# Kernel optimization log

Hardware: AMD Instinct MI355X
Metric: run time of the kernel (lower is better)

## Reference

```python
import jax, jax.numpy as jnp
import numpy as np

B, IN, H = 4096, 1024, 1024


def setup_inputs() -> dict:
    key = jax.random.key(0)
    ks = jax.random.split(key, 20)
    s_in = 1.0 / np.sqrt(IN)
    s_h = 1.0 / np.sqrt(H)
    def lin(kw, kb, fan_in, scale):
        W = jax.random.uniform(kw, (H, fan_in), jnp.float32, -scale, scale)
        b = jax.random.uniform(kb, (H,), jnp.float32, -scale, scale)
        return W, b
    Wxf, bxf = lin(ks[0], ks[1], IN, s_in)
    Whf, bhf = lin(ks[2], ks[3], H, s_h)
    Wxi, bxi = lin(ks[4], ks[5], IN, s_in)
    Whi, bhi = lin(ks[6], ks[7], H, s_h)
    Wxo, bxo = lin(ks[8], ks[9], IN, s_in)
    Who, bho = lin(ks[10], ks[11], H, s_h)
    Wxc, bxc = lin(ks[12], ks[13], IN, s_in)
    Whc, bhc = lin(ks[14], ks[15], H, s_h)
    x = jax.random.normal(ks[16], (B, IN), jnp.float32)
    c = jax.random.normal(ks[17], (B, H), jnp.float32)
    h = jax.random.normal(ks[18], (B, H), jnp.float32)
    return dict(x=x, c=c, h=h,
                Wxf=Wxf, bxf=bxf, Whf=Whf, bhf=bhf,
                Wxi=Wxi, bxi=bxi, Whi=Whi, bhi=bhi,
                Wxo=Wxo, bxo=bxo, Who=Who, bho=bho,
                Wxc=Wxc, bxc=bxc, Whc=Whc, bhc=bhc)


def reference(x, c, h,
              Wxf, bxf, Whf, bhf,
              Wxi, bxi, Whi, bhi,
              Wxo, bxo, Who, bho,
              Wxc, bxc, Whc, bhc):
    # Fuse the 8 small GEMMs into two batched GEMMs: x @ Wx^T and h @ Wh^T
    # with gate outputs concatenated along the hidden dim [f, i, o, c~].
    Wx = jnp.concatenate([Wxf, Wxi, Wxo, Wxc], axis=0)   # [4H, IN]
    Wh = jnp.concatenate([Whf, Whi, Who, Whc], axis=0)   # [4H, H]
    bx = jnp.concatenate([bxf, bxi, bxo, bxc], axis=0)   # [4H]
    bh = jnp.concatenate([bhf, bhi, bho, bhc], axis=0)   # [4H]
    gates = x @ Wx.T + h @ Wh.T + (bx + bh)              # [B, 4H]
    hs = Wxf.shape[0]
    f = jax.nn.sigmoid(gates[:, 0 * hs:1 * hs])
    i = jax.nn.sigmoid(gates[:, 1 * hs:2 * hs])
    o = jax.nn.sigmoid(gates[:, 2 * hs:3 * hs])
    ctil = jnp.tanh(gates[:, 3 * hs:4 * hs])
    ct = f * c + ctil * i
    ht = jnp.tanh(ct) * o
    return (ct, ht)
```

## Files before the change

kernel.cpp:

```cpp
#include <hip/hip_runtime.h>
#include <hip/hip_bf16.h>
#include <stdint.h>

typedef __hip_bfloat16 bf16;
typedef __attribute__((ext_vector_type(8))) short short8;
typedef __attribute__((ext_vector_type(4))) float floatx4;

#define AS1(p) ((const __attribute__((address_space(1))) void*)(p))
#define AS3(p) ((__attribute__((address_space(3))) void*)(p))

#define M_DIM 4096
#define H_DIM 1024
#define MEG   (1u << 20)
#define LDS_BUF 24576

__device__ __forceinline__ unsigned short f2bf(float f) {
    uint32_t u = __float_as_uint(f);
    uint32_t r = (u + 0x7FFFu + ((u >> 16) & 1u)) >> 16;
    return (unsigned short)r;
}

__device__ __forceinline__ float fast_sigmoid(float v) {
    return 1.0f / (1.0f + __expf(-v));
}
__device__ __forceinline__ float fast_tanh(float v) {
    return 2.0f / (1.0f + __expf(-2.0f * v)) - 1.0f;
}

__global__ __launch_bounds__(256)
void convert_to_bf16(const float* __restrict__ x, const float* __restrict__ h,
                     const float* Wxf, const float* Wxi, const float* Wxo, const float* Wxc,
                     const float* Whf, const float* Whi, const float* Who, const float* Whc,
                     unsigned short* __restrict__ ws)
{
    const uint32_t idx0 = blockIdx.x * 2048u + threadIdx.x * 8u;
    const uint32_t t = blockIdx.x >> 9;
    const float* src;
    uint32_t off;
    if (t < 4u)      { src = x; off = idx0; }
    else if (t < 8u) { src = h; off = idx0 - (4u << 20); }
    else {
        const uint32_t g = t - 8u;
        src = (g == 0) ? Wxf : (g == 1) ? Wxi : (g == 2) ? Wxo : (g == 3) ? Wxc
            : (g == 4) ? Whf : (g == 5) ? Whi : (g == 6) ? Who : Whc;
        off = idx0 & (MEG - 1u);
    }
    const float4 v0 = *(const float4*)(src + off);
    const float4 v1 = *(const float4*)(src + off + 4);
    short8 pk;
    pk[0] = (short)f2bf(v0.x); pk[1] = (short)f2bf(v0.y);
    pk[2] = (short)f2bf(v0.z); pk[3] = (short)f2bf(v0.w);
    pk[4] = (short)f2bf(v1.x); pk[5] = (short)f2bf(v1.y);
    pk[6] = (short)f2bf(v1.z); pk[7] = (short)f2bf(v1.w);
    *(short8*)(ws + idx0) = pk;
}

__global__ __launch_bounds__(512, 4)
void lstm_fused_kernel(const unsigned short* __restrict__ ws,
                       const float* __restrict__ c,
                       const float* __restrict__ bxf, const float* __restrict__ bhf,
                       const float* __restrict__ bxi, const float* __restrict__ bhi,
                       const float* __restrict__ bxo, const float* __restrict__ bho,
                       const float* __restrict__ bxc, const float* __restrict__ bhc,
                       float* __restrict__ out)
{
    __shared__ __align__(16) char lds[3 * LDS_BUF];

    const int tid  = threadIdx.x;
    const int w    = tid >> 6;
    const int lane = tid & 63;

    const int bid = blockIdx.x;
    const int mx  = bid >> 4;
    const int ny  = ((bid & 7) << 1) | ((bid >> 3) & 1);
    const int bm0 = mx * 128;
    const int bn0 = ny * 64;

    const uint32_t cg = (((uint32_t)lane & 3u) ^ (((uint32_t)lane >> 3) & 3u)) * 8u;
    const unsigned short* srcP0[3];
    const unsigned short* srcP1[3];
    uint32_t goff[3];
    uint32_t loff[3];
#pragma unroll
    for (int i = 0; i < 3; ++i) {
        const int ch = w * 3 + i;
        if (ch < 8) {
            const int row = bm0 + ch * 16 + (lane >> 2);
            srcP0[i] = ws;
            srcP1[i] = ws + (4u << 20);
            goff[i] = (uint32_t)row * 1024u + cg;
            loff[i] = (uint32_t)ch * 1024u;
        } else {
            const int b = ch - 8;
            const int g = b >> 2;
            const int n = bn0 + (b & 3) * 16 + (lane >> 2);
            srcP0[i] = ws + (8u << 20)  + (uint32_t)g * MEG;
            srcP1[i] = ws + (12u << 20) + (uint32_t)g * MEG;
            goff[i] = (uint32_t)n * 1024u + cg;
            loff[i] = 8192u + (uint32_t)b * 1024u;
        }
    }

    const int wrow  = (w & 1) * 64;
    const int wcol  = (w >> 1) * 16;
    const int lrc   = lane & 15;
    const int lquad = lane >> 4;

    const uint32_t kslot = (((uint32_t)lquad ^ (((uint32_t)lrc >> 1) & 3u))) * 8u;

    uint32_t aoff[4];
#pragma unroll
    for (int mt = 0; mt < 4; ++mt)
        aoff[mt] = (uint32_t)((wrow + mt * 16 + lrc) * 32) + kslot;
    uint32_t boff[4];
#pragma unroll
    for (int g = 0; g < 4; ++g)
        boff[g] = (uint32_t)(g * 2048 + (wcol + lrc) * 32) + kslot;

    floatx4 acc[4][4];
#pragma unroll
    for (int g = 0; g < 4; ++g)
#pragma unroll
        for (int mt = 0; mt < 4; ++mt)
            acc[g][mt] = (floatx4){0.f, 0.f, 0.f, 0.f};

    auto issue_loads = [&](int kt, uint32_t stage) {
        const int phase = kt >> 5;
        const uint32_t k0 = (uint32_t)(kt & 31) * 32u;
        const uint32_t bb = stage * LDS_BUF;
#pragma unroll
        for (int i = 0; i < 3; ++i) {
            const unsigned short* src = phase ? srcP1[i] : srcP0[i];
            __builtin_amdgcn_global_load_lds(AS1(src + goff[i] + k0),
                                             AS3(lds + bb + loff[i]), 16, 0, 0);
        }
    };
    auto compute = [&](uint32_t stage) {
        const char* base = lds + stage * LDS_BUF;
        const bf16* lA = (const bf16*)base;
        const bf16* lB = (const bf16*)(base + 8192);
        short8 afr[4];
#pragma unroll
        for (int mt = 0; mt < 4; ++mt)
            afr[mt] = *(const short8*)(lA + aoff[mt]);
#pragma unroll
        for (int g = 0; g < 4; ++g) {
            const short8 bfr = *(const short8*)(lB + boff[g]);
#pragma unroll
            for (int mt = 0; mt < 4; ++mt)
                acc[g][mt] = __builtin_amdgcn_mfma_f32_16x16x32_bf16(
                    afr[mt], bfr, acc[g][mt], 0, 0, 0);
        }
    };

    issue_loads(0, 0);
    issue_loads(1, 1);

    uint32_t s_comp = 0;
    uint32_t s_load = 2;
    for (int kt = 0; kt < 62; ++kt) {
        asm volatile("s_waitcnt vmcnt(3)\ns_barrier" ::: "memory");
        issue_loads(kt + 2, s_load);
        compute(s_comp);
        s_comp = (s_comp == 2) ? 0 : s_comp + 1;
        s_load = (s_load == 2) ? 0 : s_load + 1;
    }
    asm volatile("s_waitcnt vmcnt(3)\ns_barrier" ::: "memory");
    compute(s_comp);
    s_comp = (s_comp == 2) ? 0 : s_comp + 1;
    asm volatile("s_waitcnt vmcnt(0)\ns_barrier" ::: "memory");
    compute(s_comp);

    float* out_ct = out;
    float* out_ht = out + (size_t)M_DIM * H_DIM;
    {
        const int col = bn0 + wcol + lrc;
        const float bf_ = bxf[col] + bhf[col];
        const float bi_ = bxi[col] + bhi[col];
        const float bo_ = bxo[col] + bho[col];
        const float bc_ = bxc[col] + bhc[col];
#pragma unroll
        for (int mt = 0; mt < 4; ++mt) {
#pragma unroll
            for (int r = 0; r < 4; ++r) {
                const int row = bm0 + wrow + mt * 16 + lquad * 4 + r;
                const float gf = acc[0][mt][r] + bf_;
                const float gi = acc[1][mt][r] + bi_;
                const float go = acc[2][mt][r] + bo_;
                const float gc = acc[3][mt][r] + bc_;
                const float f    = fast_sigmoid(gf);
                const float ii   = fast_sigmoid(gi);
                const float o    = fast_sigmoid(go);
                const float ctil = fast_tanh(gc);
                const float cv   = c[(size_t)row * H_DIM + col];
                const float ctn  = f * cv + ctil * ii;
                const float htn  = fast_tanh(ctn) * o;
                out_ct[(size_t)row * H_DIM + col] = ctn;
                out_ht[(size_t)row * H_DIM + col] = htn;
            }
        }
    }
}

extern "C" void kernel_launch(void* const* d_in, const int* in_sizes, int n_in,
                              void* d_out, int out_size, void* d_ws, size_t ws_size,
                              hipStream_t stream) {
    (void)in_sizes; (void)n_in; (void)out_size; (void)ws_size;
    const float* x   = (const float*)d_in[0];
    const float* c   = (const float*)d_in[1];
    const float* h   = (const float*)d_in[2];
    const float* Wxf = (const float*)d_in[3];  const float* bxf = (const float*)d_in[4];
    const float* Whf = (const float*)d_in[5];  const float* bhf = (const float*)d_in[6];
    const float* Wxi = (const float*)d_in[7];  const float* bxi = (const float*)d_in[8];
    const float* Whi = (const float*)d_in[9];  const float* bhi = (const float*)d_in[10];
    const float* Wxo = (const float*)d_in[11]; const float* bxo = (const float*)d_in[12];
    const float* Who = (const float*)d_in[13]; const float* bho = (const float*)d_in[14];
    const float* Wxc = (const float*)d_in[15]; const float* bxc = (const float*)d_in[16];
    const float* Whc = (const float*)d_in[17]; const float* bhc = (const float*)d_in[18];
    float* out = (float*)d_out;
    unsigned short* ws = (unsigned short*)d_ws;

    convert_to_bf16<<<8192, 256, 0, stream>>>(x, h,
        Wxf, Wxi, Wxo, Wxc, Whf, Whi, Who, Whc, ws);

    lstm_fused_kernel<<<512, 512, 0, stream>>>(ws, c,
        bxf, bhf, bxi, bhi, bxo, bho, bxc, bhc, out);
}
```

Baseline: 217.0 us.

## Pre-pack bf16 operands into tile-contiguous swizzled layout for GEMM loads

```diff
diff --git a/kernel.cpp b/kernel.cpp
--- a/kernel.cpp
+++ b/kernel.cpp
@@ -28,31 +28,49 @@
 }
 
 __global__ __launch_bounds__(256)
-void convert_to_bf16(const float* __restrict__ x, const float* __restrict__ h,
-                     const float* Wxf, const float* Wxi, const float* Wxo, const float* Wxc,
-                     const float* Whf, const float* Whi, const float* Who, const float* Whc,
-                     unsigned short* __restrict__ ws)
+void pack_bf16(const float* __restrict__ x, const float* __restrict__ h,
+               const float* Wxf, const float* Wxi, const float* Wxo, const float* Wxc,
+               const float* Whf, const float* Whi, const float* Who, const float* Whc,
+               unsigned short* __restrict__ ws)
 {
-    const uint32_t idx0 = blockIdx.x * 2048u + threadIdx.x * 8u;
-    const uint32_t t = blockIdx.x >> 9;
+    const int w = threadIdx.x >> 6;
+    const int l = threadIdx.x & 63;
+    const uint32_t W = blockIdx.x * 4u + (uint32_t)w;
+
+    const uint32_t r  = (uint32_t)l >> 2;
+    const uint32_t kg = ((uint32_t)l & 3u) ^ ((r >> 1) & 3u);
+
     const float* src;
-    uint32_t off;
-    if (t < 4u)      { src = x; off = idx0; }
-    else if (t < 8u) { src = h; off = idx0 - (4u << 20); }
-    else {
-        const uint32_t g = t - 8u;
-        src = (g == 0) ? Wxf : (g == 1) ? Wxi : (g == 2) ? Wxo : (g == 3) ? Wxc
-            : (g == 4) ? Whf : (g == 5) ? Whi : (g == 6) ? Who : Whc;
-        off = idx0 & (MEG - 1u);
-    }
-    const float4 v0 = *(const float4*)(src + off);
-    const float4 v1 = *(const float4*)(src + off + 4);
+    uint32_t row, kt;
+    if (W < 16384u) {
+        const uint32_t Wa = W & 8191u;
+        const uint32_t ch = Wa & 7u;
+        kt = (Wa >> 3) & 31u;
+        const uint32_t mx = Wa >> 8;
+        src = (W < 8192u) ? x : h;
+        row = mx * 128u + ch * 16u + r;
+    } else {
+        const uint32_t V = W & 8191u;
+        kt = V & 31u;
+        uint32_t U = V >> 5;
+        const uint32_t b4 = U & 3u;
+        const uint32_t g  = (U >> 2) & 3u;
+        const uint32_t ny = U >> 4;
+        if (W < 24576u)
+            src = (g == 0) ? Wxf : (g == 1) ? Wxi : (g == 2) ? Wxo : Wxc;
+        else
+            src = (g == 0) ? Whf : (g == 1) ? Whi : (g == 2) ? Who : Whc;
+        row = ny * 64u + b4 * 16u + r;
+    }
+    const float* s = src + (size_t)row * 1024u + kt * 32u + kg * 8u;
+    const float4 v0 = *(const float4*)s;
+    const float4 v1 = *(const float4*)(s + 4);
     short8 pk;
     pk[0] = (short)f2bf(v0.x); pk[1] = (short)f2bf(v0.y);
     pk[2] = (short)f2bf(v0.z); pk[3] = (short)f2bf(v0.w);
     pk[4] = (short)f2bf(v1.x); pk[5] = (short)f2bf(v1.y);
     pk[6] = (short)f2bf(v1.z); pk[7] = (short)f2bf(v1.w);
-    *(short8*)(ws + idx0) = pk;
+    *(short8*)(ws + (size_t)W * 512u + (uint32_t)l * 8u) = pk;
 }
 
 __global__ __launch_bounds__(512, 4)
@@ -76,29 +94,34 @@
     const int bm0 = mx * 128;
     const int bn0 = ny * 64;
 
-    const uint32_t cg = (((uint32_t)lane & 3u) ^ (((uint32_t)lane >> 3) & 3u)) * 8u;
     const unsigned short* srcP0[3];
     const unsigned short* srcP1[3];
-    uint32_t goff[3];
+    uint32_t kstr[3];
     uint32_t loff[3];
 #pragma unroll
     for (int i = 0; i < 3; ++i) {
         const int ch = w * 3 + i;
         if (ch < 8) {
-            const int row = bm0 + ch * 16 + (lane >> 2);
-            srcP0[i] = ws;
-            srcP1[i] = ws + (4u << 20);
-            goff[i] = (uint32_t)row * 1024u + cg;
-            loff[i] = (uint32_t)ch * 1024u;
+            const uint32_t base = ((uint32_t)mx * 32u * 8u + (uint32_t)ch) * 512u;
+            srcP0[i] = ws + base + (uint32_t)lane * 8u;
+            srcP1[i] = srcP0[i] + (8u << 20);
+            kstr[i]  = 8u * 512u;
+            loff[i]  = (uint32_t)ch * 1024u;
         } else {
-            const int b = ch - 8;
-            const int g = b >> 2;
-            const int n = bn0 + (b & 3) * 16 + (lane >> 2);
-            srcP0[i] = ws + (8u << 20)  + (uint32_t)g * MEG;
-            srcP1[i] = ws + (12u << 20) + (uint32_t)g * MEG;
-            goff[i] = (uint32_t)n * 1024u + cg;
-            loff[i] = 8192u + (uint32_t)b * 1024u;
-        }
+            const int b  = ch - 8;
+            const uint32_t g  = (uint32_t)b >> 2;
+            const uint32_t b4 = (uint32_t)b & 3u;
+            const uint32_t base = (16384u + ((uint32_t)ny * 16u + g * 4u + b4) * 32u) * 512u;
+            srcP0[i] = ws + base + (uint32_t)lane * 8u;
+            srcP1[i] = srcP0[i] + (8192u * 512u);
+            kstr[i]  = 512u;
+            loff[i]  = 8192u + (uint32_t)b * 1024u;
+        }
+    }
+#pragma unroll
+    for (int i = 0; i < 3; ++i) {
+        const int ch = w * 3 + i;
+        if (ch < 8) srcP1[i] = srcP0[i] + 8192u * 512u;
     }
 
     const int wrow  = (w & 1) * 64;
@@ -126,13 +149,12 @@
 
     auto issue_loads = [&](int kt, uint32_t stage) {
         const int phase = kt >> 5;
-        const uint32_t k0 = (uint32_t)(kt & 31) * 32u;
+        const uint32_t kk = (uint32_t)(kt & 31);
         const uint32_t bb = stage * LDS_BUF;
 #pragma unroll
         for (int i = 0; i < 3; ++i) {
-            const unsigned short* src = phase ? srcP1[i] : srcP0[i];
-            __builtin_amdgcn_global_load_lds(AS1(src + goff[i] + k0),
-                                             AS3(lds + bb + loff[i]), 16, 0, 0);
+            const unsigned short* src = (phase ? srcP1[i] : srcP0[i]) + kk * kstr[i];
+            __builtin_amdgcn_global_load_lds(AS1(src), AS3(lds + bb + loff[i]), 16, 0, 0);
         }
     };
     auto compute = [&](uint32_t stage) {
@@ -220,7 +242,7 @@
     float* out = (float*)d_out;
     unsigned short* ws = (unsigned short*)d_ws;
 
-    convert_to_bf16<<<8192, 256, 0, stream>>>(x, h,
+    pack_bf16<<<8192, 256, 0, stream>>>(x, h,
         Wxf, Wxi, Wxo, Wxc, Whf, Whi, Who, Whc, ws);
 
     lstm_fused_kernel<<<512, 512, 0, stream>>>(ws, c,
```

Result: faster. 207.1 us (-4.6%).
